# Optimization experiments

Hardware: AMD Instinct MI355X
Metric: run time of the kernel (lower is better)

The kernel has to match this reference:

```python
import jax, jax.numpy as jnp
import numpy as np

VOCAB, EMB, H1, H2, H3, OUT = 27, 20, 32, 64, 64, 26
SEQ, BATCH = 512, 2048


def _rnn_layer(x, W_ih, W_hh, b_ih, b_hh):
    # x: (T, B, in). Elman tanh recurrence, h0 = 0.
    # Precompute input projection for all timesteps (one big GEMM).
    xi = jnp.einsum('tbi,hi->tbh', x, W_ih) + b_ih + b_hh  # (T, B, H)
    H = W_hh.shape[0]
    h0 = jnp.zeros((x.shape[1], H), dtype=x.dtype)

    def step(h, xi_t):
        h_new = jnp.tanh(xi_t + h @ W_hh.T)
        return h_new, h_new

    _, hs = jax.lax.scan(step, h0, xi)
    return hs  # (T, B, H)


def setup_inputs() -> dict:
    key = jax.random.key(0)
    ks = jax.random.split(key, 16)
    x = jax.random.randint(ks[0], (SEQ, BATCH), 0, VOCAB, dtype=jnp.int32)

    def u(k, shape, fan):
        bound = 1.0 / np.sqrt(fan)
        return jax.random.uniform(k, shape, jnp.float32, -bound, bound)

    return {
        'x': x,
        'emb': jax.random.normal(ks[1], (VOCAB, EMB), jnp.float32),
        'W_ih1': u(ks[2], (H1, EMB), H1), 'W_hh1': u(ks[3], (H1, H1), H1),
        'b_ih1': u(ks[4], (H1,), H1), 'b_hh1': u(ks[5], (H1,), H1),
        'W_ih2': u(ks[6], (H2, H1), H2), 'W_hh2': u(ks[7], (H2, H2), H2),
        'b_ih2': u(ks[8], (H2,), H2), 'b_hh2': u(ks[9], (H2,), H2),
        'W_ih3': u(ks[10], (H3, H2), H3), 'W_hh3': u(ks[11], (H3, H3), H3),
        'b_ih3': u(ks[12], (H3,), H3), 'b_hh3': u(ks[13], (H3,), H3),
        'W_fc': u(ks[14], (OUT, H3), OUT), 'b_fc': u(ks[15], (OUT,), OUT),
    }


def reference(x, emb, W_ih1, W_hh1, b_ih1, b_hh1, W_ih2, W_hh2, b_ih2, b_hh2,
              W_ih3, W_hh3, b_ih3, b_hh3, W_fc, b_fc):
    h = emb[x]                                    # (T, B, EMB) embedding lookup
    h = _rnn_layer(h, W_ih1, W_hh1, b_ih1, b_hh1)  # (T, B, 32)
    h = _rnn_layer(h, W_ih2, W_hh2, b_ih2, b_hh2)  # (T, B, 64)
    h = _rnn_layer(h, W_ih3, W_hh3, b_ih3, b_hh3)  # (T, B, 64)
    return h @ W_fc.T + b_fc                       # (T, B, 26)
```

## Files before the change

kernel.cpp:

```cpp
#include <hip/hip_runtime.h>
#include <hip/hip_bf16.h>


#define SEQ   512
#define BATCH 2048
#define OUTD  26
#define NSLOT 384
#define TBL_OFF (NSLOT*64)

#define SWZ_XOR16 0x401F

__device__ __forceinline__ int swz16i(int v) {
  return __builtin_amdgcn_ds_swizzle(v, SWZ_XOR16);
}
__device__ __forceinline__ float swz16f(float v) {
  return __int_as_float(__builtin_amdgcn_ds_swizzle(__float_as_int(v), SWZ_XOR16));
}
__device__ __forceinline__ int xor32i(int addr, int v) {
  return __builtin_amdgcn_ds_bpermute(addr, v);
}
__device__ __forceinline__ float xor32f(int addr, float v) {
  return __int_as_float(__builtin_amdgcn_ds_bpermute(addr, __float_as_int(v)));
}
__device__ __forceinline__ float bpermf(int addr, float v) {
  return __int_as_float(__builtin_amdgcn_ds_bpermute(addr, __float_as_int(v)));
}

template<int I> __device__ __forceinline__ int rotI(int v) {
  if constexpr (I == 0) return v;
  else return __builtin_amdgcn_update_dpp(0, v, 0x120 + I, 0xF, 0xF, false);
}
__device__ int rot_sw(int v, int i) {
  switch (i & 15) {
    case 0:  return rotI<0>(v);   case 1:  return rotI<1>(v);
    case 2:  return rotI<2>(v);   case 3:  return rotI<3>(v);
    case 4:  return rotI<4>(v);   case 5:  return rotI<5>(v);
    case 6:  return rotI<6>(v);   case 7:  return rotI<7>(v);
    case 8:  return rotI<8>(v);   case 9:  return rotI<9>(v);
    case 10: return rotI<10>(v);  case 11: return rotI<11>(v);
    case 12: return rotI<12>(v);  case 13: return rotI<13>(v);
    case 14: return rotI<14>(v);  case 15: return rotI<15>(v);
  }
  return v;
}

template<int I> __device__ __forceinline__ void fma_rot(float& a, float h, float w) {
  if constexpr (I == 0) {
    a = __builtin_fmaf(h, w, a);
  } else {
    asm("v_fmac_f32_dpp %0, %1, %2 row_ror:%3 row_mask:0xf bank_mask:0xf"
        : "+v"(a) : "v"(h), "v"(w), "n"(I));
  }
}

#define ROW16(A, V, B)                       \
  fma_rot<0>(A, V, wreg[(B) + 0]);           \
  fma_rot<1>(A, V, wreg[(B) + 1]);           \
  fma_rot<2>(A, V, wreg[(B) + 2]);           \
  fma_rot<3>(A, V, wreg[(B) + 3]);           \
  fma_rot<4>(A, V, wreg[(B) + 4]);           \
  fma_rot<5>(A, V, wreg[(B) + 5]);           \
  fma_rot<6>(A, V, wreg[(B) + 6]);           \
  fma_rot<7>(A, V, wreg[(B) + 7]);           \
  fma_rot<8>(A, V, wreg[(B) + 8]);           \
  fma_rot<9>(A, V, wreg[(B) + 9]);           \
  fma_rot<10>(A, V, wreg[(B) + 10]);         \
  fma_rot<11>(A, V, wreg[(B) + 11]);         \
  fma_rot<12>(A, V, wreg[(B) + 12]);         \
  fma_rot<13>(A, V, wreg[(B) + 13]);         \
  fma_rot<14>(A, V, wreg[(B) + 14]);         \
  fma_rot<15>(A, V, wreg[(B) + 15]);

#define GEMV64P(A, A2, V, V16, V32, V48, B) do { \
    ROW16(A,  V,   (B));        \
    ROW16(A2, V16, (B)+16);     \
    ROW16(A,  V32, (B)+32);     \
    ROW16(A2, V48, (B)+48);     \
  } while (0)

__device__ __forceinline__ float mul_guard(float a, float b) {
  float r;
  asm("v_mul_f32 %0, %1, %2\n\ts_nop 1" : "=v"(r) : "v"(a), "v"(b));
  return r;
}
__device__ __forceinline__ float guard_val(float x) {
  float r;
  asm("v_mov_b32 %0, %1\n\ts_nop 1" : "=v"(r) : "v"(x));
  return r;
}

__device__ __forceinline__ float tanh_u(float x) {
  x = fminf(10.f, fmaxf(-10.f, x));
  float e = __expf(-2.f * x);
  float d = 1.f + e;
  float r = __builtin_amdgcn_rcpf(d);
  r = r * (2.f - d * r);
  return (1.f - e) * r;
}
__device__ __forceinline__ float tanh_g(float x) {
  x = fminf(10.f, fmaxf(-10.f, x));
  float e = __expf(-2.f * x);
  float d = 1.f + e;
  float r = __builtin_amdgcn_rcpf(d);
  r = r * (2.f - d * r);
  return mul_guard(1.f - e, r);
}

__global__ __launch_bounds__(64) void prep_kernel(
    const float* __restrict__ emb,
    const float* __restrict__ Wih1, const float* __restrict__ Whh1,
    const float* __restrict__ bih1, const float* __restrict__ bhh1,
    const float* __restrict__ Wih2, const float* __restrict__ Whh2,
    const float* __restrict__ Wih3, const float* __restrict__ Whh3,
    const float* __restrict__ Wfc,  float* __restrict__ ws) {
  const int lane  = threadIdx.x;
  const int xaddr = ((lane ^ 32) << 2);
  const int s     = blockIdx.x;

  if (s < NSLOT) {
    const float* Wp; int ncol, row, v, p, local, colbase = 0;
    if (s < 32)       { local = s;       v = lane;      Wp = Whh1; ncol = 32; row = lane & 31; p = local >> 4; }
    else if (s < 64)  { local = s - 32;  v = lane & 31; Wp = Wih2; ncol = 32; row = lane;      p = local >> 4; }
    else if (s < 128) { local = s - 64;  v = lane;      Wp = Whh2; ncol = 64; row = lane;      p = local >> 4; }
    else if (s < 192) { local = s - 128; v = lane;      Wp = Wih3; ncol = 64; row = lane;      p = local >> 4; }
    else if (s < 256) { local = s - 192; v = lane;      Wp = Whh3; ncol = 64; row = lane;      p = local >> 4; }
    else if (s < 320) { local = s - 256; v = lane;      Wp = Wih3; ncol = 64; row = lane;      p = local >> 4; }
    else              { local = s - 320; v = lane;      Wp = Wfc;  ncol = 64; row = lane & 31;
                        p = (local >> 4) & 1; colbase = (local >> 5) * 32; }
    int i = local & 15;

    int pv;
    switch (p) {
      case 0: pv = v; break;
      case 1: pv = swz16i(v); break;
      case 2: pv = xor32i(xaddr, v); break;
      default: pv = swz16i(xor32i(xaddr, v)); break;
    }
    int pi = rot_sw(pv, i);

    float w;
    if (s >= 320) {
      int col = (pi & 31) + colbase;
      w = (row < OUTD) ? Wp[row * 64 + col] : 0.f;
    } else {
      int col = pi & (ncol - 1);
      w = Wp[row * ncol + col];
    }
    ws[(s >> 2) * 256 + lane * 4 + (s & 3)] = w;
  } else {
    int idx = (s - NSLOT) * 64 + lane;
    if (idx < 27 * 32) {
      int vv = idx >> 5, j = idx & 31;
      float acc = bih1[j] + bhh1[j];
      for (int e = 0; e < 20; ++e) acc += emb[vv * 20 + e] * Wih1[j * 20 + e];
      ws[TBL_OFF + idx] = acc;
    }
  }
}

__global__ __launch_bounds__(128, 2) void rnn_main(
    const int*   __restrict__ x,
    const float* __restrict__ bih2, const float* __restrict__ bhh2,
    const float* __restrict__ bih3, const float* __restrict__ bhh3,
    const float* __restrict__ bfc,
    const float* __restrict__ ws,   float* __restrict__ out) {
  __shared__ float tbl[27 * 32];
  __shared__ float cbuf[2][3][64];

  const int tid   = threadIdx.x;
  const int lane  = tid & 63;
  const bool wA   = (tid < 64);
  const int xaddr = ((lane ^ 32) << 2);
  const int alo   = (lane & 31) << 2;
  const int ahi   = alo + 128;
  const int jlow  = lane & 31;

  for (int idx = tid; idx < 27 * 32; idx += 128) tbl[idx] = ws[TBL_OFF + idx];

  float wreg[192];
  {
    const float4* wsv = (const float4*)ws;
    const int gbase = wA ? 0 : 48;
#pragma unroll
    for (int g = 0; g < 48; ++g) {
      float4 q = wsv[(gbase + g) * 64 + lane];
      wreg[4*g+0] = q.x; wreg[4*g+1] = q.y; wreg[4*g+2] = q.z; wreg[4*g+3] = q.w;
    }
  }
  __syncthreads();

  const int b0   = blockIdx.x * 2;
  const int bsel = b0 + (lane >> 5);

  const float beta2  = bih2[lane] + bhh2[lane];
  const float beta3  = bih3[lane] + bhh3[lane];
  const float betafc = (jlow < OUTD) ? bfc[jlow] : 0.f;

  float vh1 = 0.f, v1s = 0.f;
  float h20 = 0.f, h20a = 0.f, h20b = 0.f, h20c = 0.f;
  float h21 = 0.f, h21a = 0.f, h21b = 0.f, h21c = 0.f;
  float h30 = 0.f, h30a = 0.f, h30b = 0.f, h30c = 0.f;
  float h31 = 0.f, h31a = 0.f, h31b = 0.f, h31c = 0.f;

  int   xv_nxt = 0;
  float tblv_cur = 0.f;
  if (wA) {
    int xv0  = x[bsel];
    tblv_cur = tbl[xv0 * 32 + jlow];
    xv_nxt   = x[BATCH + bsel];
  }
  float* outbase = out + (size_t)bsel * OUTD + jlow;

#pragma unroll 1
  for (int i = 0; i <= SEQ; ++i) {
    __syncthreads();
    if (wA) {
      if (i < SEQ) {
        int tpre   = (i + 2 < SEQ) ? (i + 2) : (SEQ - 1);
        int xv_pre = x[(size_t)tpre * BATCH + bsel];

        float a1a = tblv_cur, a1b = 0.f;
        ROW16(a1a, vh1, 0);
        ROW16(a1b, v1s, 16);
        float h1n = tanh_u(a1a + a1b);

        float tblv_n = tbl[xv_nxt * 32 + jlow];
        float hb0  = bpermf(alo, h1n);
        float hb1  = bpermf(ahi, h1n);
        float v1s_n = swz16f(h1n);
        float hb0s = swz16f(hb0);
        float hb1s = swz16f(hb1);

        float a20 = beta2, a20b = 0.f, a21 = beta2, a21b = 0.f;
        ROW16(a20, hb0, 32);  ROW16(a20b, hb0s, 48);
        ROW16(a21, hb1, 32);  ROW16(a21b, hb1s, 48);
        GEMV64P(a20, a20b, h20, h20a, h20b, h20c, 64);
        GEMV64P(a21, a21b, h21, h21a, h21b, h21c, 64);
        float h2n0 = tanh_g(a20 + a20b);
        float h2n1 = tanh_u(a21 + a21b);

        float h2n0b = xor32f(xaddr, h2n0);
        float h2n0a = swz16f(h2n0);
        float h2n0c = swz16f(h2n0b);
        float h2n1b = xor32f(xaddr, h2n1);
        float h2n1a = swz16f(h2n1);
        float h2n1c = swz16f(h2n1b);

        float p0 = beta3, p0b = 0.f;
        GEMV64P(p0, p0b, h2n0, h2n0a, h2n0b, h2n0c, 128);

        cbuf[i & 1][0][lane] = h2n1;
        cbuf[i & 1][1][lane] = p0;
        cbuf[i & 1][2][lane] = p0b;

        vh1 = h1n;  v1s = v1s_n;
        h20 = h2n0; h20a = h2n0a; h20b = h2n0b; h20c = h2n0c;
        h21 = h2n1; h21a = h2n1a; h21b = h2n1b; h21c = h2n1c;
        xv_nxt = xv_pre; tblv_cur = tblv_n;
      }
    } else {
      if (i > 0) {
        const int rb = (i - 1) & 1;
        float h2n1 = cbuf[rb][0][lane];
        float p0   = cbuf[rb][1][lane];
        float p0b  = cbuf[rb][2][lane];

        float a30 = 0.f, a30b = 0.f, a31 = beta3, a31b = 0.f;
        GEMV64P(a30, a30b, h30, h30a, h30b, h30c, 0);
        GEMV64P(a31, a31b, h31, h31a, h31b, h31c, 0);

        float h2n1b = xor32f(xaddr, h2n1);
        float h2n1a = swz16f(h2n1);
        float h2n1c = swz16f(h2n1b);
        GEMV64P(a31, a31b, h2n1, h2n1a, h2n1b, h2n1c, 64);

        float h3n0 = tanh_u((p0 + p0b) + (a30 + a30b));
        float h3n1 = tanh_u(a31 + a31b);

        float h3n0b = xor32f(xaddr, h3n0);
        float h3n0a = swz16f(h3n0);
        float h3n0c = swz16f(h3n0b);
        float h3n1b = xor32f(xaddr, h3n1);
        float h3n1a = swz16f(h3n1);
        float h3n1c = swz16f(h3n1b);

        float vm0  = guard_val((lane < 32) ? h3n0  : h3n1b);
        float vm1  = guard_val((lane < 32) ? h3n0b : h3n1 );
        float vm0s = swz16f(vm0);
        float vm1s = swz16f(vm1);
        float af = betafc, afb = 0.f;
        ROW16(af,  vm0,  128);  ROW16(afb, vm0s, 144);
        ROW16(af,  vm1,  160);  ROW16(afb, vm1s, 176);
        if (jlow < OUTD) outbase[(size_t)(i - 1) * (BATCH * OUTD)] = af + afb;

        h30 = h3n0; h30a = h3n0a; h30b = h3n0b; h30c = h3n0c;
        h31 = h3n1; h31a = h3n1a; h31b = h3n1b; h31c = h3n1c;
      }
    }
  }
}

extern "C" void kernel_launch(void* const* d_in, const int* in_sizes, int n_in,
                              void* d_out, int out_size, void* d_ws, size_t ws_size,
                              hipStream_t stream) {
  const int*   x    = (const int*)  d_in[0];
  const float* emb  = (const float*)d_in[1];
  const float* Wih1 = (const float*)d_in[2];
  const float* Whh1 = (const float*)d_in[3];
  const float* bih1 = (const float*)d_in[4];
  const float* bhh1 = (const float*)d_in[5];
  const float* Wih2 = (const float*)d_in[6];
  const float* Whh2 = (const float*)d_in[7];
  const float* bih2 = (const float*)d_in[8];
  const float* bhh2 = (const float*)d_in[9];
  const float* Wih3 = (const float*)d_in[10];
  const float* Whh3 = (const float*)d_in[11];
  const float* bih3 = (const float*)d_in[12];
  const float* bhh3 = (const float*)d_in[13];
  const float* Wfc  = (const float*)d_in[14];
  const float* bfc  = (const float*)d_in[15];
  float* ws  = (float*)d_ws;
  float* out = (float*)d_out;

  prep_kernel<<<NSLOT + 14, 64, 0, stream>>>(emb, Wih1, Whh1, bih1, bhh1,
                                             Wih2, Whh2, Wih3, Whh3, Wfc, ws);
  rnn_main<<<BATCH / 2, 128, 0, stream>>>(x, bih2, bhh2, bih3, bhh3, bfc, ws, out);
}
```

Baseline: 856.8 us.

## Interleave DPP FMA chains across four accumulators and replace swizzle chains with direct bpermutes

The rotated-FMA GEMV chains are reordered so four independent accumulators advance in lockstep, which breaks the long serial dependency through each accumulator and lets DPP FMAs issue back to back. The dependent swizzle-after-bpermute shuffles become independent ds_bpermute calls with precomputed xor-16/32/48 addresses, shortening the cross-lane latency chain. Wave A now reduces the layer-3 partial before the handoff, so the LDS buffer holds a float2 instead of three floats. In exchange there are more LDS permute instructions and more live accumulators.

```diff
diff --git a/kernel.cpp b/kernel.cpp
--- a/kernel.cpp
+++ b/kernel.cpp
@@ -13,14 +13,8 @@
 __device__ __forceinline__ int swz16i(int v) {
   return __builtin_amdgcn_ds_swizzle(v, SWZ_XOR16);
 }
-__device__ __forceinline__ float swz16f(float v) {
-  return __int_as_float(__builtin_amdgcn_ds_swizzle(__float_as_int(v), SWZ_XOR16));
-}
 __device__ __forceinline__ int xor32i(int addr, int v) {
   return __builtin_amdgcn_ds_bpermute(addr, v);
-}
-__device__ __forceinline__ float xor32f(int addr, float v) {
-  return __int_as_float(__builtin_amdgcn_ds_bpermute(addr, __float_as_int(v)));
 }
 __device__ __forceinline__ float bpermf(int addr, float v) {
   return __int_as_float(__builtin_amdgcn_ds_bpermute(addr, __float_as_int(v)));
@@ -53,30 +47,35 @@
   }
 }
 
-#define ROW16(A, V, B)                       \
-  fma_rot<0>(A, V, wreg[(B) + 0]);           \
-  fma_rot<1>(A, V, wreg[(B) + 1]);           \
-  fma_rot<2>(A, V, wreg[(B) + 2]);           \
-  fma_rot<3>(A, V, wreg[(B) + 3]);           \
-  fma_rot<4>(A, V, wreg[(B) + 4]);           \
-  fma_rot<5>(A, V, wreg[(B) + 5]);           \
-  fma_rot<6>(A, V, wreg[(B) + 6]);           \
-  fma_rot<7>(A, V, wreg[(B) + 7]);           \
-  fma_rot<8>(A, V, wreg[(B) + 8]);           \
-  fma_rot<9>(A, V, wreg[(B) + 9]);           \
-  fma_rot<10>(A, V, wreg[(B) + 10]);         \
-  fma_rot<11>(A, V, wreg[(B) + 11]);         \
-  fma_rot<12>(A, V, wreg[(B) + 12]);         \
-  fma_rot<13>(A, V, wreg[(B) + 13]);         \
-  fma_rot<14>(A, V, wreg[(B) + 14]);         \
-  fma_rot<15>(A, V, wreg[(B) + 15]);
-
-#define GEMV64P(A, A2, V, V16, V32, V48, B) do { \
-    ROW16(A,  V,   (B));        \
-    ROW16(A2, V16, (B)+16);     \
-    ROW16(A,  V32, (B)+32);     \
-    ROW16(A2, V48, (B)+48);     \
-  } while (0)
+#define I4(i, A0,V0,B0, A1,V1,B1, A2,V2,B2, A3,V3,B3) \
+  fma_rot<(i)>(A0, V0, wreg[(B0)+(i)]); \
+  fma_rot<(i)>(A1, V1, wreg[(B1)+(i)]); \
+  fma_rot<(i)>(A2, V2, wreg[(B2)+(i)]); \
+  fma_rot<(i)>(A3, V3, wreg[(B3)+(i)]);
+
+#define R16_I4(A0,V0,B0, A1,V1,B1, A2,V2,B2, A3,V3,B3) \
+  I4(0, A0,V0,B0, A1,V1,B1, A2,V2,B2, A3,V3,B3) \
+  I4(1, A0,V0,B0, A1,V1,B1, A2,V2,B2, A3,V3,B3) \
+  I4(2, A0,V0,B0, A1,V1,B1, A2,V2,B2, A3,V3,B3) \
+  I4(3, A0,V0,B0, A1,V1,B1, A2,V2,B2, A3,V3,B3) \
+  I4(4, A0,V0,B0, A1,V1,B1, A2,V2,B2, A3,V3,B3) \
+  I4(5, A0,V0,B0, A1,V1,B1, A2,V2,B2, A3,V3,B3) \
+  I4(6, A0,V0,B0, A1,V1,B1, A2,V2,B2, A3,V3,B3) \
+  I4(7, A0,V0,B0, A1,V1,B1, A2,V2,B2, A3,V3,B3) \
+  I4(8, A0,V0,B0, A1,V1,B1, A2,V2,B2, A3,V3,B3) \
+  I4(9, A0,V0,B0, A1,V1,B1, A2,V2,B2, A3,V3,B3) \
+  I4(10, A0,V0,B0, A1,V1,B1, A2,V2,B2, A3,V3,B3) \
+  I4(11, A0,V0,B0, A1,V1,B1, A2,V2,B2, A3,V3,B3) \
+  I4(12, A0,V0,B0, A1,V1,B1, A2,V2,B2, A3,V3,B3) \
+  I4(13, A0,V0,B0, A1,V1,B1, A2,V2,B2, A3,V3,B3) \
+  I4(14, A0,V0,B0, A1,V1,B1, A2,V2,B2, A3,V3,B3) \
+  I4(15, A0,V0,B0, A1,V1,B1, A2,V2,B2, A3,V3,B3)
+
+#define L1_I4(k) \
+  fma_rot<(k)>(a1a, vh1, wreg[(k)]); \
+  fma_rot<(k)+8>(a1c, vh1, wreg[8+(k)]); \
+  fma_rot<(k)>(a1b, v1s, wreg[16+(k)]); \
+  fma_rot<(k)+8>(a1d, v1s, wreg[24+(k)]);
 
 __device__ __forceinline__ float mul_guard(float a, float b) {
   float r;
@@ -165,15 +164,19 @@
     const float* __restrict__ bfc,
     const float* __restrict__ ws,   float* __restrict__ out) {
   __shared__ float tbl[27 * 32];
-  __shared__ float cbuf[2][3][64];
+  __shared__ float2 cbuf[2][64];
 
   const int tid   = threadIdx.x;
   const int lane  = tid & 63;
   const bool wA   = (tid < 64);
-  const int xaddr = ((lane ^ 32) << 2);
+  const int jlow  = lane & 31;
+  const int a16   = (lane ^ 16) << 2;
+  const int a32   = (lane ^ 32) << 2;
+  const int a48   = (lane ^ 48) << 2;
   const int alo   = (lane & 31) << 2;
   const int ahi   = alo + 128;
-  const int jlow  = lane & 31;
+  const int alo16 = ((lane & 31) ^ 16) << 2;
+  const int ahi16 = alo16 + 128;
 
   for (int idx = tid; idx < 27 * 32; idx += 128) tbl[idx] = ws[TBL_OFF + idx];
 
@@ -219,82 +222,78 @@
         int tpre   = (i + 2 < SEQ) ? (i + 2) : (SEQ - 1);
         int xv_pre = x[(size_t)tpre * BATCH + bsel];
 
-        float a1a = tblv_cur, a1b = 0.f;
-        ROW16(a1a, vh1, 0);
-        ROW16(a1b, v1s, 16);
-        float h1n = tanh_u(a1a + a1b);
-
+        float a1a = tblv_cur, a1b = 0.f, a1c = 0.f, a1d = 0.f;
+        L1_I4(0) L1_I4(1) L1_I4(2) L1_I4(3)
+        L1_I4(4) L1_I4(5) L1_I4(6) L1_I4(7)
+        float h1n = tanh_u((a1a + a1c) + (a1b + a1d));
+
+        float hb0   = bpermf(alo,   h1n);
+        float hb1   = bpermf(ahi,   h1n);
+        float hb0s  = bpermf(alo16, h1n);
+        float hb1s  = bpermf(ahi16, h1n);
+        float v1s_n = bpermf(a16,   h1n);
         float tblv_n = tbl[xv_nxt * 32 + jlow];
-        float hb0  = bpermf(alo, h1n);
-        float hb1  = bpermf(ahi, h1n);
-        float v1s_n = swz16f(h1n);
-        float hb0s = swz16f(hb0);
-        float hb1s = swz16f(hb1);
 
         float a20 = beta2, a20b = 0.f, a21 = beta2, a21b = 0.f;
-        ROW16(a20, hb0, 32);  ROW16(a20b, hb0s, 48);
-        ROW16(a21, hb1, 32);  ROW16(a21b, hb1s, 48);
-        GEMV64P(a20, a20b, h20, h20a, h20b, h20c, 64);
-        GEMV64P(a21, a21b, h21, h21a, h21b, h21c, 64);
+        R16_I4(a20, h20,  64, a20b, h20a,  80, a21, h21,  64, a21b, h21a,  80)
+        R16_I4(a20, h20b, 96, a20b, h20c, 112, a21, h21b, 96, a21b, h21c, 112)
+        R16_I4(a20, hb0,  32, a20b, hb0s,  48, a21, hb1,  32, a21b, hb1s,  48)
+
         float h2n0 = tanh_g(a20 + a20b);
+        float h2n0a = bpermf(a16, h2n0);
+        float h2n0x = bpermf(a32, h2n0);
+        float h2n0c = bpermf(a48, h2n0);
         float h2n1 = tanh_u(a21 + a21b);
-
-        float h2n0b = xor32f(xaddr, h2n0);
-        float h2n0a = swz16f(h2n0);
-        float h2n0c = swz16f(h2n0b);
-        float h2n1b = xor32f(xaddr, h2n1);
-        float h2n1a = swz16f(h2n1);
-        float h2n1c = swz16f(h2n1b);
-
-        float p0 = beta3, p0b = 0.f;
-        GEMV64P(p0, p0b, h2n0, h2n0a, h2n0b, h2n0c, 128);
-
-        cbuf[i & 1][0][lane] = h2n1;
-        cbuf[i & 1][1][lane] = p0;
-        cbuf[i & 1][2][lane] = p0b;
+        float h2n1a = bpermf(a16, h2n1);
+        float h2n1x = bpermf(a32, h2n1);
+        float h2n1c = bpermf(a48, h2n1);
+
+        float p0 = beta3, p1 = 0.f, p2 = 0.f, p3 = 0.f;
+        R16_I4(p0, h2n0, 128, p1, h2n0a, 144, p2, h2n0x, 160, p3, h2n0c, 176)
+        float ps = (p0 + p1) + (p2 + p3);
+
+        cbuf[i & 1][lane] = make_float2(h2n1, ps);
 
         vh1 = h1n;  v1s = v1s_n;
-        h20 = h2n0; h20a = h2n0a; h20b = h2n0b; h20c = h2n0c;
-        h21 = h2n1; h21a = h2n1a; h21b = h2n1b; h21c = h2n1c;
+        h20 = h2n0; h20a = h2n0a; h20b = h2n0x; h20c = h2n0c;
+        h21 = h2n1; h21a = h2n1a; h21b = h2n1x; h21c = h2n1c;
         xv_nxt = xv_pre; tblv_cur = tblv_n;
       }
     } else {
       if (i > 0) {
-        const int rb = (i - 1) & 1;
-        float h2n1 = cbuf[rb][0][lane];
-        float p0   = cbuf[rb][1][lane];
-        float p0b  = cbuf[rb][2][lane];
+        float2 c = cbuf[(i - 1) & 1][lane];
 
         float a30 = 0.f, a30b = 0.f, a31 = beta3, a31b = 0.f;
-        GEMV64P(a30, a30b, h30, h30a, h30b, h30c, 0);
-        GEMV64P(a31, a31b, h31, h31a, h31b, h31c, 0);
-
-        float h2n1b = xor32f(xaddr, h2n1);
-        float h2n1a = swz16f(h2n1);
-        float h2n1c = swz16f(h2n1b);
-        GEMV64P(a31, a31b, h2n1, h2n1a, h2n1b, h2n1c, 64);
-
-        float h3n0 = tanh_u((p0 + p0b) + (a30 + a30b));
-        float h3n1 = tanh_u(a31 + a31b);
-
-        float h3n0b = xor32f(xaddr, h3n0);
-        float h3n0a = swz16f(h3n0);
-        float h3n0c = swz16f(h3n0b);
-        float h3n1b = xor32f(xaddr, h3n1);
-        float h3n1a = swz16f(h3n1);
-        float h3n1c = swz16f(h3n1b);
-
-        float vm0  = guard_val((lane < 32) ? h3n0  : h3n1b);
-        float vm1  = guard_val((lane < 32) ? h3n0b : h3n1 );
-        float vm0s = swz16f(vm0);
-        float vm1s = swz16f(vm1);
-        float af = betafc, afb = 0.f;
-        ROW16(af,  vm0,  128);  ROW16(afb, vm0s, 144);
-        ROW16(af,  vm1,  160);  ROW16(afb, vm1s, 176);
-        if (jlow < OUTD) outbase[(size_t)(i - 1) * (BATCH * OUTD)] = af + afb;
-
-        h30 = h3n0; h30a = h3n0a; h30b = h3n0b; h30c = h3n0c;
-        h31 = h3n1; h31a = h3n1a; h31b = h3n1b; h31c = h3n1c;
+        R16_I4(a30, h30,  0, a30b, h30a, 16, a31, h31,  0, a31b, h31a, 16)
+        R16_I4(a30, h30b, 32, a30b, h30c, 48, a31, h31b, 32, a31b, h31c, 48)
+
+        float h2n1 = c.x;
+        float h2n1a = bpermf(a16, h2n1);
+        float h2n1x = bpermf(a32, h2n1);
+        float h2n1c = bpermf(a48, h2n1);
+        float h3n0 = tanh_u(c.y + (a30 + a30b));
+        float q0 = 0.f, q1 = 0.f, q2 = 0.f, q3 = 0.f;
+        R16_I4(q0, h2n1, 64, q1, h2n1a, 80, q2, h2n1x, 96, q3, h2n1c, 112)
+        float h3n1 = tanh_u(((a31 + a31b) + (q0 + q1)) + (q2 + q3));
+
+        float h3n0a = bpermf(a16, h3n0);
+        float h3n0x = bpermf(a32, h3n0);
+        float h3n0c = bpermf(a48, h3n0);
+        float h3n1a = bpermf(a16, h3n1);
+        float h3n1x = bpermf(a32, h3n1);
+        float h3n1c = bpermf(a48, h3n1);
+
+        float vm0  = guard_val((lane < 32) ? h3n0  : h3n1x);
+        float vm1  = guard_val((lane < 32) ? h3n0x : h3n1 );
+        float vm0s = guard_val((lane < 32) ? h3n0a : h3n1c);
+        float vm1s = guard_val((lane < 32) ? h3n0c : h3n1a);
+        float af = betafc, afb = 0.f, af2 = 0.f, afb2 = 0.f;
+        R16_I4(af, vm0, 128, afb, vm0s, 144, af2, vm1, 160, afb2, vm1s, 176)
+        float ov = (af + afb) + (af2 + afb2);
+        if (jlow < OUTD) outbase[(size_t)(i - 1) * (BATCH * OUTD)] = ov;
+
+        h30 = h3n0; h30a = h3n0a; h30b = h3n0x; h30c = h3n0c;
+        h31 = h3n1; h31a = h3n1a; h31b = h3n1x; h31c = h3n1c;
       }
     }
   }
```

Result: no change. 847.0 us (-1.1%).
